# Optimization experiments

Measured on AMD Instinct MI355X. Metric: run time of the kernel, lower is better.

The kernel has to match this reference:

```python
import jax, jax.numpy as jnp
import numpy as np

B, S, D, H, DFF = 4, 2048, 1024, 16, 4096
HD = D // H  # head_dim = 64


def rmsnorm(x, scale, eps=1e-6):
    var = jnp.mean(jnp.square(x), axis=-1, keepdims=True)
    return x * jax.lax.rsqrt(var + eps) * scale


def setup_inputs() -> dict:
    key = jax.random.key(0)
    ks = jax.random.split(key, 16)
    s = 1.0 / np.sqrt(D)
    inp = {
        "x": jax.random.normal(ks[0], (B, S, D), jnp.float32),
        "wq": jax.random.normal(ks[1], (D, D), jnp.float32) * s,
        "bq": jnp.zeros((D,), jnp.float32),
        "wk": jax.random.normal(ks[2], (D, D), jnp.float32) * s,
        "bk": jnp.zeros((D,), jnp.float32),
        "wv": jax.random.normal(ks[3], (D, D), jnp.float32) * s,
        "bv": jnp.zeros((D,), jnp.float32),
        "wbeta": jax.random.normal(ks[4], (D, H), jnp.float32) * s,
        "bbeta": jnp.zeros((H,), jnp.float32),
        "wo": jax.random.normal(ks[5], (D, D), jnp.float32) * s,
        "bo": jnp.zeros((D,), jnp.float32),
        "w1": jax.random.normal(ks[6], (D, DFF), jnp.float32) * s,
        "b1": jnp.zeros((DFF,), jnp.float32),
        "w2": jax.random.normal(ks[7], (DFF, D), jnp.float32) * (1.0 / np.sqrt(DFF)),
        "b2": jnp.zeros((D,), jnp.float32),
        "ln1_scale": jnp.ones((D,), jnp.float32),
        "ln2_scale": jnp.ones((D,), jnp.float32),
    }
    return inp


def gdn_attention(x, wq, bq, wk, bk, wv, bv, wbeta, bbeta, wo, bo):
    b, s, _ = x.shape
    q = (x @ wq + bq).reshape(b, s, H, HD)
    k = (x @ wk + bk).reshape(b, s, H, HD)
    v = (x @ wv + bv).reshape(b, s, H, HD)
    k = k / (jnp.linalg.norm(k, axis=-1, keepdims=True) + 1e-6)
    beta = jax.nn.sigmoid(x @ wbeta + bbeta)[..., None]  # (b, s, H, 1)

    # time-major for scan: (s, b, H, ...)
    q = jnp.transpose(q, (1, 0, 2, 3))
    k = jnp.transpose(k, (1, 0, 2, 3))
    v = jnp.transpose(v, (1, 0, 2, 3))
    beta = jnp.transpose(beta, (1, 0, 2, 3))

    def _step(Sm, inputs):
        q_t, k_t, v_t, beta_t = inputs
        Sk = jnp.einsum('bhde,bhe->bhd', Sm, k_t)
        delta = v_t - Sk
        Sm = Sm + beta_t[..., None] * jnp.einsum('bhd,bhe->bhde', delta, k_t)
        o_t = jnp.einsum('bhde,bhe->bhd', Sm, q_t)
        return Sm, o_t

    S0 = jnp.zeros((b, H, HD, HD), x.dtype)
    _, outputs = jax.lax.scan(_step, S0, (q, k, v, beta))
    outputs = jnp.transpose(outputs, (1, 0, 2, 3)).reshape(b, s, D)
    return outputs @ wo + bo


def reference(x, wq, bq, wk, bk, wv, bv, wbeta, bbeta, wo, bo,
              w1, b1, w2, b2, ln1_scale, ln2_scale):
    residual = x
    h = rmsnorm(x, ln1_scale)
    h = gdn_attention(h, wq, bq, wk, bk, wv, bv, wbeta, bbeta, wo, bo)
    x = h + residual
    residual = x
    h = rmsnorm(x, ln2_scale)
    h = jax.nn.gelu(h @ w1 + b1) @ w2 + b2
    return h + residual
```

## Files before the change

kernel.cpp:

```cpp
#include <hip/hip_runtime.h>

#define DEV __device__ __forceinline__

typedef short bf16x8 __attribute__((ext_vector_type(8)));
typedef float f32x4 __attribute__((ext_vector_type(4)));
typedef unsigned int uint;

#define SBAR()   asm volatile("s_barrier" ::: "memory")
#define WAITV(n) asm volatile("s_waitcnt vmcnt(" #n ")" ::: "memory")
#define WAITL()  asm volatile("s_waitcnt lgkmcnt(0)" ::: "memory")

DEV unsigned short f2b(float f) {
    uint u = __float_as_uint(f);
    u += 0x7fffu + ((u >> 16) & 1u);
    return (unsigned short)(u >> 16);
}
DEV uint packbf2(float a, float b) { return (uint)f2b(a) | ((uint)f2b(b) << 16); }
DEV float b2f(unsigned short s) { return __uint_as_float(((uint)s) << 16); }
DEV float b2f_lo(uint u) { return __uint_as_float(u << 16); }
DEV float b2f_hi(uint u) { return __uint_as_float(u & 0xffff0000u); }

DEV void async_cp16(const void* g, void* l) {
    __builtin_amdgcn_global_load_lds(
        (const __attribute__((address_space(1))) unsigned int*)g,
        (__attribute__((address_space(3))) unsigned int*)l, 16, 0, 0);
}

DEV float quad_sum(float x) {
    x += __int_as_float(__builtin_amdgcn_update_dpp(0, __float_as_int(x), 0xB1, 0xF, 0xF, true));
    x += __int_as_float(__builtin_amdgcn_update_dpp(0, __float_as_int(x), 0x4E, 0xF, 0xF, true));
    return x;
}

DEV float gelu_f(float u) {
    float p = u + 0.044715f * u * u * u;
    float e = __expf(-1.5957691216f * p);
    return __fdividef(u, 1.f + e);
}

DEV void dec8(uint4 p, float* o) {
    o[0] = b2f_lo(p.x); o[1] = b2f_hi(p.x); o[2] = b2f_lo(p.y); o[3] = b2f_hi(p.y);
    o[4] = b2f_lo(p.z); o[5] = b2f_hi(p.z); o[6] = b2f_lo(p.w); o[7] = b2f_hi(p.w);
}

__global__ __launch_bounds__(256) void transpose_cast_k(
    const float* __restrict__ in, unsigned short* __restrict__ out, int K, int N)
{
    __shared__ float tile[32][33];
    const int k0 = blockIdx.x * 32, n0 = blockIdx.y * 32;
    const int tx = threadIdx.x & 31, ty = threadIdx.x >> 5;
#pragma unroll
    for (int i = 0; i < 32; i += 8) {
        int n = n0 + tx;
        tile[ty + i][tx] = (n < N) ? in[(size_t)(k0 + ty + i) * N + n] : 0.0f;
    }
    __syncthreads();
#pragma unroll
    for (int i = 0; i < 32; i += 8) {
        out[(size_t)(n0 + ty + i) * K + (k0 + tx)] = f2b(tile[tx][ty + i]);
    }
}

__global__ void build_bias_k(const float* __restrict__ bq, const float* __restrict__ bk,
                             const float* __restrict__ bv, const float* __restrict__ bb,
                             float* __restrict__ outb)
{
    int i = blockIdx.x * 256 + threadIdx.x;
    if (i >= 3328) return;
    float v = 0.f;
    if (i < 1024)      v = bq[i];
    else if (i < 2048) v = bk[i - 1024];
    else if (i < 3072) v = bv[i - 2048];
    else if (i < 3088) v = bb[i - 3072];
    outb[i] = v;
}

__global__ __launch_bounds__(256) void rmsnorm_cast_k(
    const float* __restrict__ x, const float* __restrict__ scale,
    unsigned short* __restrict__ out)
{
    const int row = blockIdx.x;
    const int t = threadIdx.x;
    const float4 v = *(const float4*)(x + (size_t)row * 1024 + t * 4);
    float ss = v.x * v.x + v.y * v.y + v.z * v.z + v.w * v.w;
#pragma unroll
    for (int off = 1; off < 64; off <<= 1) ss += __shfl_xor(ss, off);
    __shared__ float wsum[4];
    if ((t & 63) == 0) wsum[t >> 6] = ss;
    __syncthreads();
    const float tot = wsum[0] + wsum[1] + wsum[2] + wsum[3];
    const float inv = rsqrtf(tot * (1.0f / 1024.0f) + 1e-6f);
    const float4 sc = *(const float4*)(scale + t * 4);
    uint lo = (uint)f2b(v.x * inv * sc.x) | ((uint)f2b(v.y * inv * sc.y) << 16);
    uint hi = (uint)f2b(v.z * inv * sc.z) | ((uint)f2b(v.w * inv * sc.w) << 16);
    uint2 pkd; pkd.x = lo; pkd.y = hi;
    *(uint2*)(out + (size_t)row * 1024 + t * 4) = pkd;
}

template <bool GELU, bool GUARD>
__global__ __launch_bounds__(512, 2) void gemm256(
    const unsigned short* __restrict__ A, const unsigned short* __restrict__ BT,
    const float* __restrict__ bias, unsigned short* __restrict__ C,
    int Nstride, int Nreal, int K)
{
    __shared__ __align__(16) unsigned short As[4][256 * 32];
    __shared__ __align__(16) unsigned short Bs[4][256 * 32];
    const int tid = threadIdx.x;
    const int wid = tid >> 6;
    const int lane = tid & 63;
    const int l16 = lane & 15, quad = lane >> 4;
    const int wm = wid & 1, wn = wid >> 1;
    const int m0 = blockIdx.x << 8, n0 = blockIdx.y << 8;

    const int srow = (wid << 5) + (lane >> 2);
    const int scol = ((lane & 3) ^ ((lane >> 3) & 3)) << 3;
    const unsigned short* Ag = A + (size_t)(m0 + srow) * K + scol;
    const unsigned short* Bg = BT + (size_t)(n0 + srow) * K + scol;
    const size_t rstep16 = (size_t)16 * K;
    const int ldst = wid << 10;

    f32x4 acc[8][4];
#pragma unroll
    for (int i = 0; i < 8; i++)
#pragma unroll
        for (int j = 0; j < 4; j++) acc[i][j] = (f32x4)0.f;

    const int ksw = (quad ^ ((l16 >> 1) & 3)) << 3;
    const int aoff = ((wm << 7) + l16) * 32 + ksw;
    const int boff = ((wn << 6) + l16) * 32 + ksw;

    const int nt = K >> 5;
    async_cp16(Ag, &As[0][ldst]);
    async_cp16(Ag + rstep16, &As[0][ldst + 512]);
    async_cp16(Bg, &Bs[0][ldst]);
    async_cp16(Bg + rstep16, &Bs[0][ldst + 512]);
    async_cp16(Ag + 32, &As[1][ldst]);
    async_cp16(Ag + 32 + rstep16, &As[1][ldst + 512]);
    async_cp16(Bg + 32, &Bs[1][ldst]);
    async_cp16(Bg + 32 + rstep16, &Bs[1][ldst + 512]);
    WAITV(4);
    SBAR();

    for (int tb = 0; tb < nt; tb += 4) {
#pragma unroll
        for (int u = 0; u < 4; ++u) {
            const int t = tb + u;
            const int pb = (u + 2) & 3;
            const bool st = (t + 2) < nt;
            const size_t kpre = (size_t)(t + 2) << 5;
            bf16x8 af[8], bfr[4];
#pragma unroll
            for (int mi = 0; mi < 8; mi++) af[mi] = *(const bf16x8*)&As[u][aoff + mi * 512];
#pragma unroll
            for (int ni = 0; ni < 4; ni++) bfr[ni] = *(const bf16x8*)&Bs[u][boff + ni * 512];
            if (st) {
                async_cp16(Ag + kpre, &As[pb][ldst]);
                async_cp16(Ag + kpre + rstep16, &As[pb][ldst + 512]);
                async_cp16(Bg + kpre, &Bs[pb][ldst]);
                async_cp16(Bg + kpre + rstep16, &Bs[pb][ldst + 512]);
                WAITV(4);
            } else {
                WAITV(0);
            }
            SBAR();
            __builtin_amdgcn_s_setprio(1);
#pragma unroll
            for (int mi = 0; mi < 8; mi++)
#pragma unroll
                for (int ni = 0; ni < 4; ni++)
                    acc[mi][ni] = __builtin_amdgcn_mfma_f32_16x16x32_bf16(af[mi], bfr[ni], acc[mi][ni], 0, 0, 0);
            __builtin_amdgcn_s_setprio(0);
            SBAR();
        }
    }

    float bv[4];
    const int ccol = n0 + (wn << 6) + l16;
#pragma unroll
    for (int ni = 0; ni < 4; ni++) bv[ni] = bias[ccol + ni * 16];
#pragma unroll
    for (int mi = 0; mi < 8; mi++) {
        const int row = m0 + (wm << 7) + mi * 16 + (quad << 2);
#pragma unroll
        for (int r = 0; r < 4; r++) {
            unsigned short* Crow = C + (size_t)(row + r) * Nstride + ccol;
#pragma unroll
            for (int ni = 0; ni < 4; ni++) {
                float v = acc[mi][ni][r] + bv[ni];
                if (GELU) v = gelu_f(v);
                if (!GUARD || (ccol + ni * 16) < Nreal) Crow[ni * 16] = f2b(v);
            }
        }
    }
}

template <bool ADD>
__global__ __launch_bounds__(512, 2) void gemm128n256(
    const unsigned short* __restrict__ A, const unsigned short* __restrict__ BT,
    const float* __restrict__ bias, const float* __restrict__ add,
    float* __restrict__ C, int N, int K)
{
    __shared__ __align__(16) unsigned short As[4][128 * 32];
    __shared__ __align__(16) unsigned short Bs[4][256 * 32];
    const int tid = threadIdx.x;
    const int wid = tid >> 6;
    const int lane = tid & 63;
    const int l16 = lane & 15, quad = lane >> 4;
    const int wm = wid & 1, wn = wid >> 1;
    const int m0 = blockIdx.x << 7, n0 = blockIdx.y << 8;

    const int arow = (wid << 4) + (lane >> 2);
    const int brow = (wid << 5) + (lane >> 2);
    const int scol = ((lane & 3) ^ ((lane >> 3) & 3)) << 3;
    const unsigned short* Ag = A + (size_t)(m0 + arow) * K + scol;
    const unsigned short* Bg = BT + (size_t)(n0 + brow) * K + scol;
    const size_t rstep16 = (size_t)16 * K;
    const int lda = wid << 9;
    const int ldb = wid << 10;

    f32x4 acc[4][4];
#pragma unroll
    for (int i = 0; i < 4; i++)
#pragma unroll
        for (int j = 0; j < 4; j++) acc[i][j] = (f32x4)0.f;

    const int ksw = (quad ^ ((l16 >> 1) & 3)) << 3;
    const int aoff = ((wm << 6) + l16) * 32 + ksw;
    const int boff = ((wn << 6) + l16) * 32 + ksw;

    const int nt = K >> 5;
    async_cp16(Ag, &As[0][lda]);
    async_cp16(Bg, &Bs[0][ldb]);
    async_cp16(Bg + rstep16, &Bs[0][ldb + 512]);
    async_cp16(Ag + 32, &As[1][lda]);
    async_cp16(Bg + 32, &Bs[1][ldb]);
    async_cp16(Bg + 32 + rstep16, &Bs[1][ldb + 512]);
    WAITV(3);
    SBAR();

    for (int tb = 0; tb < nt; tb += 4) {
#pragma unroll
        for (int u = 0; u < 4; ++u) {
            const int t = tb + u;
            const int pb = (u + 2) & 3;
            const bool st = (t + 2) < nt;
            const size_t kpre = (size_t)(t + 2) << 5;
            bf16x8 af[4], bfr[4];
#pragma unroll
            for (int mi = 0; mi < 4; mi++) af[mi] = *(const bf16x8*)&As[u][aoff + mi * 512];
#pragma unroll
            for (int ni = 0; ni < 4; ni++) bfr[ni] = *(const bf16x8*)&Bs[u][boff + ni * 512];
            if (st) {
                async_cp16(Ag + kpre, &As[pb][lda]);
                async_cp16(Bg + kpre, &Bs[pb][ldb]);
                async_cp16(Bg + kpre + rstep16, &Bs[pb][ldb + 512]);
                WAITV(3);
            } else {
                WAITV(0);
            }
            SBAR();
            __builtin_amdgcn_s_setprio(1);
#pragma unroll
            for (int mi = 0; mi < 4; mi++)
#pragma unroll
                for (int ni = 0; ni < 4; ni++)
                    acc[mi][ni] = __builtin_amdgcn_mfma_f32_16x16x32_bf16(af[mi], bfr[ni], acc[mi][ni], 0, 0, 0);
            __builtin_amdgcn_s_setprio(0);
            SBAR();
        }
    }

    const int ccol = n0 + (wn << 6) + l16;
    float bv[4];
#pragma unroll
    for (int ni = 0; ni < 4; ni++) bv[ni] = bias[ccol + ni * 16];
#pragma unroll
    for (int mi = 0; mi < 4; mi++) {
        const int row = m0 + (wm << 6) + mi * 16 + (quad << 2);
#pragma unroll
        for (int r = 0; r < 4; r++) {
#pragma unroll
            for (int ni = 0; ni < 4; ni++) {
                size_t idx = (size_t)(row + r) * N + ccol + ni * 16;
                float v = acc[mi][ni][r] + bv[ni];
                if (ADD) v += add[idx];
                C[idx] = v;
            }
        }
    }
}


__global__ __launch_bounds__(256) void gdn_prep(
    unsigned short* __restrict__ qkv, unsigned short* __restrict__ Wg,
    unsigned short* __restrict__ ZTg, unsigned short* __restrict__ KTg)
{
    const int chunk = blockIdx.x, bh = blockIdx.y;
    const int b = bh >> 4, h = bh & 15;
    __shared__ float Ks[64 * 68];
    __shared__ float Ws[64 * 65];
    __shared__ float Zs[64 * 65];
    __shared__ float Asl[64 * 65];
    __shared__ float bs[64];
    const int tid = threadIdx.x;
    const int t = tid >> 2, c = tid & 3;
    unsigned short* rowp = qkv + (size_t)(b * 2048 + chunk * 64 + t) * 3200;

    float kn[16];
    {
        uint4 ka = *(const uint4*)(rowp + 1024 + h * 64 + 16 * c);
        uint4 kb = *(const uint4*)(rowp + 1024 + h * 64 + 16 * c + 8);
        dec8(ka, kn); dec8(kb, kn + 8);
    }
    float ss = 0.f;
#pragma unroll
    for (int j = 0; j < 16; j++) ss += kn[j] * kn[j];
    ss = quad_sum(ss);
    const float inv = 1.f / (sqrtf(ss) + 1e-6f);
#pragma unroll
    for (int j = 0; j < 16; j++) kn[j] *= inv;
#pragma unroll
    for (int j = 0; j < 16; j++) Ks[t * 68 + 16 * c + j] = kn[j];
    {
        uint4 p0, p1;
        p0.x = packbf2(kn[0], kn[1]);  p0.y = packbf2(kn[2], kn[3]);
        p0.z = packbf2(kn[4], kn[5]);  p0.w = packbf2(kn[6], kn[7]);
        p1.x = packbf2(kn[8], kn[9]);  p1.y = packbf2(kn[10], kn[11]);
        p1.z = packbf2(kn[12], kn[13]); p1.w = packbf2(kn[14], kn[15]);
        *(uint4*)(rowp + 1024 + h * 64 + 16 * c) = p0;
        *(uint4*)(rowp + 1024 + h * 64 + 16 * c + 8) = p1;
    }
    if (c == 0) bs[t] = 1.f / (1.f + __expf(-b2f(rowp[3072 + h])));
    __syncthreads();

    const float beta = bs[t];
#pragma unroll
    for (int j = 0; j < 16; j++) Ws[t * 65 + 16 * c + j] = beta * kn[j];
    {
        float vv[16];
        uint4 va = *(const uint4*)(rowp + 2048 + h * 64 + 16 * c);
        uint4 vb = *(const uint4*)(rowp + 2048 + h * 64 + 16 * c + 8);
        dec8(va, vv); dec8(vb, vv + 8);
#pragma unroll
        for (int j = 0; j < 16; j++) Zs[t * 65 + 16 * c + j] = beta * vv[j];
    }
    __syncthreads();

    {
        const int tt = tid >> 4, sx = tid & 15;
        float dm[4][4];
#pragma unroll
        for (int i = 0; i < 4; i++)
#pragma unroll
            for (int j = 0; j < 4; j++) dm[i][j] = 0.f;
        for (int d = 0; d < 64; d++) {
            float kt[4], ksv[4];
#pragma unroll
            for (int i = 0; i < 4; i++) kt[i] = Ks[(4 * tt + i) * 68 + d];
#pragma unroll
            for (int j = 0; j < 4; j++) ksv[j] = Ks[(4 * sx + j) * 68 + d];
#pragma unroll
            for (int i = 0; i < 4; i++)
#pragma unroll
                for (int j = 0; j < 4; j++) dm[i][j] += kt[i] * ksv[j];
        }
#pragma unroll
        for (int i = 0; i < 4; i++)
#pragma unroll
            for (int j = 0; j < 4; j++) {
                int T = 4 * tt + i, S_ = 4 * sx + j;
                Asl[T * 65 + S_] = (S_ < T) ? bs[T] * dm[i][j] : 0.f;
            }
    }
    __syncthreads();

    {
        const int wid = tid >> 6, lane = tid & 63;
        for (int qi = 0; qi < 4; qi++) {
            if (qi > 0) {
                const int tb = qi * 16 + wid * 4;
                float aw[4], az[4];
#pragma unroll
                for (int i = 0; i < 4; i++) { aw[i] = Ws[(tb + i) * 65 + lane]; az[i] = Zs[(tb + i) * 65 + lane]; }
                for (int s = 0; s < qi * 16; s++) {
                    float wsv = Ws[s * 65 + lane], zsv = Zs[s * 65 + lane];
#pragma unroll
                    for (int i = 0; i < 4; i++) {
                        float a = Asl[(tb + i) * 65 + s];
                        aw[i] -= a * wsv; az[i] -= a * zsv;
                    }
                }
#pragma unroll
                for (int i = 0; i < 4; i++) { Ws[(tb + i) * 65 + lane] = aw[i]; Zs[(tb + i) * 65 + lane] = az[i]; }
            }
            __syncthreads();
            if (wid == 0) {
                for (int T = qi * 16; T < qi * 16 + 16; T++) {
                    float a_ = Ws[T * 65 + lane];
                    for (int s = qi * 16; s < T; s++) a_ -= Asl[T * 65 + s] * Ws[s * 65 + lane];
                    Ws[T * 65 + lane] = a_;
                }
            } else if (wid == 1) {
                for (int T = qi * 16; T < qi * 16 + 16; T++) {
                    float a_ = Zs[T * 65 + lane];
                    for (int s = qi * 16; s < T; s++) a_ -= Asl[T * 65 + s] * Zs[s * 65 + lane];
                    Zs[T * 65 + lane] = a_;
                }
            }
            __syncthreads();
        }
    }

    const size_t cbase = ((size_t)bh * 32 + chunk) * 4096;
    {
#pragma unroll
        for (int half = 0; half < 2; half++) {
            uint4 w4;
            w4.x = packbf2(Ws[t * 65 + 16 * c + half * 8 + 0], Ws[t * 65 + 16 * c + half * 8 + 1]);
            w4.y = packbf2(Ws[t * 65 + 16 * c + half * 8 + 2], Ws[t * 65 + 16 * c + half * 8 + 3]);
            w4.z = packbf2(Ws[t * 65 + 16 * c + half * 8 + 4], Ws[t * 65 + 16 * c + half * 8 + 5]);
            w4.w = packbf2(Ws[t * 65 + 16 * c + half * 8 + 6], Ws[t * 65 + 16 * c + half * 8 + 7]);
            *(uint4*)(Wg + cbase + (size_t)((2 * c + half) * 64 + t) * 8) = w4;
        }
    }
    {
        const int jj = tid >> 2, tq = tid & 3;
#pragma unroll
        for (int half = 0; half < 2; half++) {
            uint4 z4;
            int i0 = half * 8;
            z4.x = packbf2(Zs[(16 * tq + i0 + 0) * 65 + jj], Zs[(16 * tq + i0 + 1) * 65 + jj]);
            z4.y = packbf2(Zs[(16 * tq + i0 + 2) * 65 + jj], Zs[(16 * tq + i0 + 3) * 65 + jj]);
            z4.z = packbf2(Zs[(16 * tq + i0 + 4) * 65 + jj], Zs[(16 * tq + i0 + 5) * 65 + jj]);
            z4.w = packbf2(Zs[(16 * tq + i0 + 6) * 65 + jj], Zs[(16 * tq + i0 + 7) * 65 + jj]);
            *(uint4*)(ZTg + cbase + (size_t)((2 * tq + half) * 64 + jj) * 8) = z4;
        }
    }
    {
        const int dd = tid >> 2, tq = tid & 3;
#pragma unroll
        for (int half = 0; half < 2; half++) {
            uint4 k4;
            int i0 = half * 8;
            k4.x = packbf2(Ks[(16 * tq + i0 + 0) * 68 + dd], Ks[(16 * tq + i0 + 1) * 68 + dd]);
            k4.y = packbf2(Ks[(16 * tq + i0 + 2) * 68 + dd], Ks[(16 * tq + i0 + 3) * 68 + dd]);
            k4.z = packbf2(Ks[(16 * tq + i0 + 4) * 68 + dd], Ks[(16 * tq + i0 + 5) * 68 + dd]);
            k4.w = packbf2(Ks[(16 * tq + i0 + 6) * 68 + dd], Ks[(16 * tq + i0 + 7) * 68 + dd]);
            *(uint4*)(KTg + cbase + (size_t)((2 * tq + half) * 64 + dd) * 8) = k4;
        }
    }
}

__global__ __launch_bounds__(256, 1) void gdn_prop_mfma(
    const unsigned short* __restrict__ Wg, const unsigned short* __restrict__ KTg,
    const unsigned short* __restrict__ ZTg, unsigned short* __restrict__ Sg,
    unsigned short* __restrict__ YTg)
{
    const int bh = blockIdx.x;
    __shared__ unsigned short WbU[2][4096];
    __shared__ unsigned short KTbU[2][4096];
    __shared__ unsigned short ZTbU[2][4096];
    __shared__ unsigned short SbU[4096];
    const int tid = threadIdx.x;
    const int wid = tid >> 6;
    const int lane = tid & 63;
    const int l16 = lane & 15, quad = lane >> 4;

    f32x4 Sacc[4];
#pragma unroll
    for (int dt = 0; dt < 4; dt++) Sacc[dt] = (f32x4)0.f;

    {
        const size_t cb0 = ((size_t)bh * 32) * 4096;
#pragma unroll
        for (int p = 0; p < 2; p++) {
            const int n = wid * 2 + p;
            async_cp16(Wg + cb0 + n * 512 + lane * 8, &WbU[0][n * 512]);
            async_cp16(KTg + cb0 + n * 512 + lane * 8, &KTbU[0][n * 512]);
            async_cp16(ZTg + cb0 + n * 512 + lane * 8, &ZTbU[0][n * 512]);
        }
    }
    WAITV(0);
    SBAR();

    for (int ch = 0; ch < 32; ch++) {
        const int cur = ch & 1, nxt = cur ^ 1;
        const size_t cbase = ((size_t)bh * 32 + ch) * 4096;
        unsigned short* Wb  = WbU[cur];
        unsigned short* KTb = KTbU[cur];
        unsigned short* ZTb = ZTbU[cur];

        if (ch + 1 < 32) {
            const size_t cbn = cbase + 4096;
#pragma unroll
            for (int p = 0; p < 2; p++) {
                const int n = wid * 2 + p;
                async_cp16(Wg + cbn + n * 512 + lane * 8, &WbU[nxt][n * 512]);
                async_cp16(KTg + cbn + n * 512 + lane * 8, &KTbU[nxt][n * 512]);
                async_cp16(ZTg + cbn + n * 512 + lane * 8, &ZTbU[nxt][n * 512]);
            }
        }
#pragma unroll
        for (int dt = 0; dt < 4; dt++) {
#pragma unroll
            for (int r = 0; r < 4; r++) {
                const int j = wid * 16 + quad * 4 + r;
                SbU[((2 * dt + (l16 >> 3)) * 64 + j) * 8 + (l16 & 7)] = f2b(Sacc[dt][r]);
            }
        }
        WAITL();
        SBAR();

        {
            uint4 sa0 = *(const uint4*)&SbU[tid * 16];
            uint4 sa1 = *(const uint4*)&SbU[tid * 16 + 8];
            *(uint4*)(Sg + cbase + tid * 16) = sa0;
            *(uint4*)(Sg + cbase + tid * 16 + 8) = sa1;
        }

        f32x4 t1[4];
#pragma unroll
        for (int tt = 0; tt < 4; tt++) t1[tt] = (f32x4)0.f;
#pragma unroll
        for (int kh = 0; kh < 2; kh++) {
            const int g = kh * 4 + quad;
            bf16x8 afr = *(const bf16x8*)&SbU[(g * 64 + wid * 16 + l16) * 8];
#pragma unroll
            for (int tt = 0; tt < 4; tt++) {
                bf16x8 bfr = *(const bf16x8*)&Wb[(g * 64 + tt * 16 + l16) * 8];
                t1[tt] = __builtin_amdgcn_mfma_f32_16x16x32_bf16(afr, bfr, t1[tt], 0, 0, 0);
            }
        }
#pragma unroll
        for (int tt = 0; tt < 4; tt++) {
            const int t = tt * 16 + l16;
            const int gb = (t >> 3) * 64;
            unsigned short ybf[4];
#pragma unroll
            for (int r = 0; r < 4; r++) {
                const int j = wid * 16 + quad * 4 + r;
                const float z = b2f(ZTb[(gb + j) * 8 + (t & 7)]);
                ybf[r] = f2b(z - t1[tt][r]);
            }
#pragma unroll
            for (int r = 0; r < 4; r++) {
                const int j = wid * 16 + quad * 4 + r;
                ZTb[(gb + j) * 8 + (t & 7)] = ybf[r];
            }
        }
#pragma unroll
        for (int kh = 0; kh < 2; kh++) {
            const int g = kh * 4 + quad;
            bf16x8 afr = *(const bf16x8*)&ZTb[(g * 64 + wid * 16 + l16) * 8];
#pragma unroll
            for (int dt = 0; dt < 4; dt++) {
                bf16x8 bfr = *(const bf16x8*)&KTb[(g * 64 + dt * 16 + l16) * 8];
                Sacc[dt] = __builtin_amdgcn_mfma_f32_16x16x32_bf16(afr, bfr, Sacc[dt], 0, 0, 0);
            }
        }
#pragma unroll
        for (int pp = 0; pp < 2; pp++) {
            const int p = lane * 2 + pp;
            const int g = p >> 4, jj = p & 15;
            const int off = (g * 64 + wid * 16 + jj) * 8;
            uint4 yv = *(const uint4*)&ZTb[off];
            *(uint4*)(YTg + cbase + off) = yv;
        }
        WAITV(0);
        SBAR();
    }
}

__global__ __launch_bounds__(256) void gdn_out(
    const unsigned short* __restrict__ qkv, const unsigned short* __restrict__ YTg,
    const unsigned short* __restrict__ Sg, unsigned short* __restrict__ attn)
{
    const int chunk = blockIdx.x, bh = blockIdx.y;
    const int b = bh >> 4, h = bh & 15;
    __shared__ unsigned short QbU[8 * 516];
    __shared__ unsigned short KbU[8 * 516];
    __shared__ unsigned short StU[8 * 516];
    __shared__ unsigned short YtU[8 * 516];
    __shared__ unsigned short MhU[8 * 516];
    __shared__ unsigned short MlU[8 * 516];
    const int tid = threadIdx.x;
    const int wid = tid >> 6, lane = tid & 63;
    const int l16 = lane & 15, quad = lane >> 4;
    const size_t cbase = ((size_t)bh * 32 + chunk) * 4096;

    {
        const int t = tid >> 2, c = tid & 3;
        const unsigned short* rowp = qkv + (size_t)(b * 2048 + chunk * 64 + t) * 3200;
        uint4 qa = *(const uint4*)(rowp + h * 64 + 16 * c);
        uint4 qb = *(const uint4*)(rowp + h * 64 + 16 * c + 8);
        uint4 ka = *(const uint4*)(rowp + 1024 + h * 64 + 16 * c);
        uint4 kb = *(const uint4*)(rowp + 1024 + h * 64 + 16 * c + 8);
        *(uint4*)&QbU[(2 * c) * 516 + t * 8]     = qa;
        *(uint4*)&QbU[(2 * c + 1) * 516 + t * 8] = qb;
        *(uint4*)&KbU[(2 * c) * 516 + t * 8]     = ka;
        *(uint4*)&KbU[(2 * c + 1) * 516 + t * 8] = kb;
        const int g = tid >> 5, row = (tid * 2) & 63;
        uint4 s0 = *(const uint4*)(Sg + cbase + tid * 16);
        uint4 s1 = *(const uint4*)(Sg + cbase + tid * 16 + 8);
        *(uint4*)&StU[g * 516 + row * 8]       = s0;
        *(uint4*)&StU[g * 516 + (row + 1) * 8] = s1;
        uint4 y0 = *(const uint4*)(YTg + cbase + tid * 16);
        uint4 y1 = *(const uint4*)(YTg + cbase + tid * 16 + 8);
        *(uint4*)&YtU[g * 516 + row * 8]       = y0;
        *(uint4*)&YtU[g * 516 + (row + 1) * 8] = y1;
    }
    __syncthreads();

    f32x4 m[4], o[4];
#pragma unroll
    for (int i = 0; i < 4; i++) { m[i] = (f32x4)0.f; o[i] = (f32x4)0.f; }

#pragma unroll
    for (int kh = 0; kh < 2; kh++) {
        const int g = kh * 4 + quad;
        bf16x8 afr = *(const bf16x8*)&QbU[g * 516 + (wid * 16 + l16) * 8];
#pragma unroll
        for (int st = 0; st < 4; st++) {
            bf16x8 bk = *(const bf16x8*)&KbU[g * 516 + (st * 16 + l16) * 8];
            m[st] = __builtin_amdgcn_mfma_f32_16x16x32_bf16(afr, bk, m[st], 0, 0, 0);
        }
#pragma unroll
        for (int jt = 0; jt < 4; jt++) {
            bf16x8 bs_ = *(const bf16x8*)&StU[g * 516 + (jt * 16 + l16) * 8];
            o[jt] = __builtin_amdgcn_mfma_f32_16x16x32_bf16(afr, bs_, o[jt], 0, 0, 0);
        }
    }

#pragma unroll
    for (int st = 0; st < 4; st++) {
#pragma unroll
        for (int r = 0; r < 4; r++) {
            const int t = wid * 16 + quad * 4 + r;
            const int s = st * 16 + l16;
            float v = (s <= t) ? m[st][r] : 0.f;
            unsigned short hi = f2b(v);
            unsigned short lo = f2b(v - b2f(hi));
            const int addr = (s >> 3) * 516 + t * 8 + (s & 7);
            MhU[addr] = hi;
            MlU[addr] = lo;
        }
    }
    __syncthreads();

#pragma unroll
    for (int kh = 0; kh < 2; kh++) {
        const int g = kh * 4 + quad;
        bf16x8 ah = *(const bf16x8*)&MhU[g * 516 + (wid * 16 + l16) * 8];
        bf16x8 al = *(const bf16x8*)&MlU[g * 516 + (wid * 16 + l16) * 8];
#pragma unroll
        for (int jt = 0; jt < 4; jt++) {
            bf16x8 by = *(const bf16x8*)&YtU[g * 516 + (jt * 16 + l16) * 8];
            o[jt] = __builtin_amdgcn_mfma_f32_16x16x32_bf16(ah, by, o[jt], 0, 0, 0);
            o[jt] = __builtin_amdgcn_mfma_f32_16x16x32_bf16(al, by, o[jt], 0, 0, 0);
        }
    }

#pragma unroll
    for (int jt = 0; jt < 4; jt++) {
#pragma unroll
        for (int r = 0; r < 4; r++) {
            const int t = wid * 16 + quad * 4 + r;
            attn[(size_t)(b * 2048 + chunk * 64 + t) * 1024 + h * 64 + jt * 16 + l16] = f2b(o[jt][r]);
        }
    }
}

static constexpr size_t OFF_H     = 0;
static constexpr size_t OFF_WQKVT = OFF_H + 16777216;
static constexpr size_t OFF_WOT   = OFF_WQKVT + 6553600;
static constexpr size_t OFF_W1T   = OFF_WOT + 2097152;
static constexpr size_t OFF_W2T   = OFF_W1T + 8388608;
static constexpr size_t OFF_BIAS  = OFF_W2T + 8388608;
static constexpr size_t OFF_QKV   = OFF_BIAS + 16384;
static constexpr size_t OFF_ATTN  = OFF_QKV + 67108864;
static constexpr size_t OFF_Y1    = OFF_ATTN + 16777216;
static constexpr size_t OFF_WG    = OFF_Y1 + 33554432;
static constexpr size_t OFF_YG    = OFF_WG + 16777216;

extern "C" void kernel_launch(void* const* d_in, const int* in_sizes, int n_in,
                              void* d_out, int out_size, void* d_ws, size_t ws_size,
                              hipStream_t stream)
{
    const float* x     = (const float*)d_in[0];
    const float* wq    = (const float*)d_in[1];
    const float* bq    = (const float*)d_in[2];
    const float* wk    = (const float*)d_in[3];
    const float* bk    = (const float*)d_in[4];
    const float* wv    = (const float*)d_in[5];
    const float* bv    = (const float*)d_in[6];
    const float* wbeta = (const float*)d_in[7];
    const float* bbeta = (const float*)d_in[8];
    const float* wo    = (const float*)d_in[9];
    const float* bo    = (const float*)d_in[10];
    const float* w1    = (const float*)d_in[11];
    const float* b1    = (const float*)d_in[12];
    const float* w2    = (const float*)d_in[13];
    const float* b2    = (const float*)d_in[14];
    const float* ln1   = (const float*)d_in[15];
    const float* ln2   = (const float*)d_in[16];

    char* ws = (char*)d_ws;
    unsigned short* hbuf  = (unsigned short*)(ws + OFF_H);
    unsigned short* Sg    = (unsigned short*)(ws + OFF_H);
    unsigned short* wqkvT = (unsigned short*)(ws + OFF_WG);
    unsigned short* woT   = (unsigned short*)(ws + OFF_WOT);
    unsigned short* w1T   = (unsigned short*)(ws + OFF_W1T);
    unsigned short* w2T   = (unsigned short*)(ws + OFF_W2T);
    float*          biasc = (float*)(ws + OFF_BIAS);
    unsigned short* qkvU  = (unsigned short*)(ws + OFF_QKV);
    unsigned short* gbuf  = (unsigned short*)(ws + OFF_QKV);
    unsigned short* attn  = (unsigned short*)(ws + OFF_ATTN);
    float*          y1    = (float*)(ws + OFF_Y1);
    unsigned short* ZTg   = (unsigned short*)(ws + OFF_Y1);
    unsigned short* KTg   = (unsigned short*)(ws + OFF_Y1 + 16777216);
    unsigned short* Wg    = (unsigned short*)(ws + OFF_WG);
    unsigned short* YTg   = (unsigned short*)(ws + OFF_YG);
    float*          out   = (float*)d_out;

    transpose_cast_k<<<dim3(32, 32), 256, 0, stream>>>(wq, wqkvT,               1024, 1024);
    transpose_cast_k<<<dim3(32, 32), 256, 0, stream>>>(wk, wqkvT + 1024 * 1024, 1024, 1024);
    transpose_cast_k<<<dim3(32, 32), 256, 0, stream>>>(wv, wqkvT + 2048 * 1024, 1024, 1024);
    transpose_cast_k<<<dim3(32, 8),  256, 0, stream>>>(wbeta, wqkvT + 3072 * 1024, 1024, 16);
    transpose_cast_k<<<dim3(32, 32), 256, 0, stream>>>(wo, woT, 1024, 1024);
    transpose_cast_k<<<dim3(32, 128), 256, 0, stream>>>(w1, w1T, 1024, 4096);
    transpose_cast_k<<<dim3(128, 32), 256, 0, stream>>>(w2, w2T, 4096, 1024);
    build_bias_k<<<13, 256, 0, stream>>>(bq, bk, bv, bbeta, biasc);

    rmsnorm_cast_k<<<8192, 256, 0, stream>>>(x, ln1, hbuf);
    gemm256<false, true><<<dim3(32, 13), 512, 0, stream>>>(hbuf, wqkvT, biasc, qkvU, 3200, 3200, 1024);
    gdn_prep<<<dim3(32, 64), 256, 0, stream>>>(qkvU, Wg, ZTg, KTg);
    gdn_prop_mfma<<<64, 256, 0, stream>>>(Wg, KTg, ZTg, Sg, YTg);
    gdn_out<<<dim3(32, 64), 256, 0, stream>>>(qkvU, YTg, Sg, attn);
    gemm128n256<true><<<dim3(64, 4), 512, 0, stream>>>(attn, woT, bo, x, y1, 1024, 1024);
    rmsnorm_cast_k<<<8192, 256, 0, stream>>>(y1, ln2, hbuf);
    gemm256<true, false><<<dim3(32, 16), 512, 0, stream>>>(hbuf, w1T, b1, gbuf, 4096, 4096, 1024);
    gemm128n256<true><<<dim3(64, 4), 512, 0, stream>>>(gbuf, w2T, b2, y1, out, 1024, 4096);
}
```

Measured before the change: 596.1 us.

## Switch GEMMs to double-buffered LDS and 128x128 tiles for output projections

The large GEMM goes from a 4-stage, 2-ahead async prefetch pipeline to a 2-stage double buffer: it issues the next tile's loads before computing and waits for them after the MFMAs. This halves LDS use, which may let more blocks fit per CU. The wo and w2 GEMMs are replaced by a 256-thread kernel with 128x128 tiles, doubling the grid to 512 blocks for better CU coverage. In exchange, prefetch distance is shorter, so load latency is exposed more easily, and each iteration still has a barrier.

After: 647.4 us. +8.6%, slower.

```diff
diff --git a/kernel.cpp b/kernel.cpp
--- a/kernel.cpp
+++ b/kernel.cpp
@@ -103,8 +103,8 @@
     const float* __restrict__ bias, unsigned short* __restrict__ C,
     int Nstride, int Nreal, int K)
 {
-    __shared__ __align__(16) unsigned short As[4][256 * 32];
-    __shared__ __align__(16) unsigned short Bs[4][256 * 32];
+    __shared__ __align__(16) unsigned short As[2][256 * 32];
+    __shared__ __align__(16) unsigned short Bs[2][256 * 32];
     const int tid = threadIdx.x;
     const int wid = tid >> 6;
     const int lane = tid & 63;
@@ -134,35 +134,26 @@
     async_cp16(Ag + rstep16, &As[0][ldst + 512]);
     async_cp16(Bg, &Bs[0][ldst]);
     async_cp16(Bg + rstep16, &Bs[0][ldst + 512]);
-    async_cp16(Ag + 32, &As[1][ldst]);
-    async_cp16(Ag + 32 + rstep16, &As[1][ldst + 512]);
-    async_cp16(Bg + 32, &Bs[1][ldst]);
-    async_cp16(Bg + 32 + rstep16, &Bs[1][ldst + 512]);
-    WAITV(4);
+    WAITV(0);
     SBAR();
 
-    for (int tb = 0; tb < nt; tb += 4) {
-#pragma unroll
-        for (int u = 0; u < 4; ++u) {
+    for (int tb = 0; tb < nt; tb += 2) {
+#pragma unroll
+        for (int u = 0; u < 2; ++u) {
             const int t = tb + u;
-            const int pb = (u + 2) & 3;
-            const bool st = (t + 2) < nt;
-            const size_t kpre = (size_t)(t + 2) << 5;
+            const int nb = u ^ 1;
+            if (t + 1 < nt) {
+                const size_t kp = (size_t)(t + 1) << 5;
+                async_cp16(Ag + kp, &As[nb][ldst]);
+                async_cp16(Ag + kp + rstep16, &As[nb][ldst + 512]);
+                async_cp16(Bg + kp, &Bs[nb][ldst]);
+                async_cp16(Bg + kp + rstep16, &Bs[nb][ldst + 512]);
+            }
             bf16x8 af[8], bfr[4];
 #pragma unroll
             for (int mi = 0; mi < 8; mi++) af[mi] = *(const bf16x8*)&As[u][aoff + mi * 512];
 #pragma unroll
             for (int ni = 0; ni < 4; ni++) bfr[ni] = *(const bf16x8*)&Bs[u][boff + ni * 512];
-            if (st) {
-                async_cp16(Ag + kpre, &As[pb][ldst]);
-                async_cp16(Ag + kpre + rstep16, &As[pb][ldst + 512]);
-                async_cp16(Bg + kpre, &Bs[pb][ldst]);
-                async_cp16(Bg + kpre + rstep16, &Bs[pb][ldst + 512]);
-                WAITV(4);
-            } else {
-                WAITV(0);
-            }
-            SBAR();
             __builtin_amdgcn_s_setprio(1);
 #pragma unroll
             for (int mi = 0; mi < 8; mi++)
@@ -170,6 +161,7 @@
                 for (int ni = 0; ni < 4; ni++)
                     acc[mi][ni] = __builtin_amdgcn_mfma_f32_16x16x32_bf16(af[mi], bfr[ni], acc[mi][ni], 0, 0, 0);
             __builtin_amdgcn_s_setprio(0);
+            WAITV(0);
             SBAR();
         }
     }
@@ -195,28 +187,26 @@
 }
 
 template <bool ADD>
-__global__ __launch_bounds__(512, 2) void gemm128n256(
+__global__ __launch_bounds__(256, 2) void gemm128s(
     const unsigned short* __restrict__ A, const unsigned short* __restrict__ BT,
     const float* __restrict__ bias, const float* __restrict__ add,
     float* __restrict__ C, int N, int K)
 {
-    __shared__ __align__(16) unsigned short As[4][128 * 32];
-    __shared__ __align__(16) unsigned short Bs[4][256 * 32];
+    __shared__ __align__(16) unsigned short As[2][128 * 32];
+    __shared__ __align__(16) unsigned short Bs[2][128 * 32];
     const int tid = threadIdx.x;
     const int wid = tid >> 6;
     const int lane = tid & 63;
     const int l16 = lane & 15, quad = lane >> 4;
     const int wm = wid & 1, wn = wid >> 1;
-    const int m0 = blockIdx.x << 7, n0 = blockIdx.y << 8;
-
-    const int arow = (wid << 4) + (lane >> 2);
-    const int brow = (wid << 5) + (lane >> 2);
-    const int scol = ((lane & 3) ^ ((lane >> 3) & 3)) << 3;
-    const unsigned short* Ag = A + (size_t)(m0 + arow) * K + scol;
-    const unsigned short* Bg = BT + (size_t)(n0 + brow) * K + scol;
-    const size_t rstep16 = (size_t)16 * K;
-    const int lda = wid << 9;
-    const int ldb = wid << 10;
+    const int m0 = blockIdx.x << 7, n0 = blockIdx.y << 7;
+
+    const int srow = tid >> 2;
+    const int scol = ((tid & 3) ^ ((tid >> 3) & 3)) << 3;
+    const unsigned short* Ag = A + (size_t)(m0 + srow) * K + scol;
+    const unsigned short* Bg = BT + (size_t)(n0 + srow) * K + scol;
+    const size_t rstep64 = (size_t)64 * K;
+    const int ldst = wid << 9;
 
     f32x4 acc[4][4];
 #pragma unroll
@@ -229,36 +219,30 @@
     const int boff = ((wn << 6) + l16) * 32 + ksw;
 
     const int nt = K >> 5;
-    async_cp16(Ag, &As[0][lda]);
-    async_cp16(Bg, &Bs[0][ldb]);
-    async_cp16(Bg + rstep16, &Bs[0][ldb + 512]);
-    async_cp16(Ag + 32, &As[1][lda]);
-    async_cp16(Bg + 32, &Bs[1][ldb]);
-    async_cp16(Bg + 32 + rstep16, &Bs[1][ldb + 512]);
-    WAITV(3);
+    async_cp16(Ag, &As[0][ldst]);
+    async_cp16(Ag + rstep64, &As[0][2048 + ldst]);
+    async_cp16(Bg, &Bs[0][ldst]);
+    async_cp16(Bg + rstep64, &Bs[0][2048 + ldst]);
+    WAITV(0);
     SBAR();
 
-    for (int tb = 0; tb < nt; tb += 4) {
-#pragma unroll
-        for (int u = 0; u < 4; ++u) {
+    for (int tb = 0; tb < nt; tb += 2) {
+#pragma unroll
+        for (int u = 0; u < 2; ++u) {
             const int t = tb + u;
-            const int pb = (u + 2) & 3;
-            const bool st = (t + 2) < nt;
-            const size_t kpre = (size_t)(t + 2) << 5;
+            const int nb = u ^ 1;
+            if (t + 1 < nt) {
+                const size_t kp = (size_t)(t + 1) << 5;
+                async_cp16(Ag + kp, &As[nb][ldst]);
+                async_cp16(Ag + kp + rstep64, &As[nb][2048 + ldst]);
+                async_cp16(Bg + kp, &Bs[nb][ldst]);
+                async_cp16(Bg + kp + rstep64, &Bs[nb][2048 + ldst]);
+            }
             bf16x8 af[4], bfr[4];
 #pragma unroll
             for (int mi = 0; mi < 4; mi++) af[mi] = *(const bf16x8*)&As[u][aoff + mi * 512];
 #pragma unroll
             for (int ni = 0; ni < 4; ni++) bfr[ni] = *(const bf16x8*)&Bs[u][boff + ni * 512];
-            if (st) {
-                async_cp16(Ag + kpre, &As[pb][lda]);
-                async_cp16(Bg + kpre, &Bs[pb][ldb]);
-                async_cp16(Bg + kpre + rstep16, &Bs[pb][ldb + 512]);
-                WAITV(3);
-            } else {
-                WAITV(0);
-            }
-            SBAR();
             __builtin_amdgcn_s_setprio(1);
 #pragma unroll
             for (int mi = 0; mi < 4; mi++)
@@ -266,6 +250,7 @@
                 for (int ni = 0; ni < 4; ni++)
                     acc[mi][ni] = __builtin_amdgcn_mfma_f32_16x16x32_bf16(af[mi], bfr[ni], acc[mi][ni], 0, 0, 0);
             __builtin_amdgcn_s_setprio(0);
+            WAITV(0);
             SBAR();
         }
     }
@@ -736,8 +721,8 @@
     gdn_prep<<<dim3(32, 64), 256, 0, stream>>>(qkvU, Wg, ZTg, KTg);
     gdn_prop_mfma<<<64, 256, 0, stream>>>(Wg, KTg, ZTg, Sg, YTg);
     gdn_out<<<dim3(32, 64), 256, 0, stream>>>(qkvU, YTg, Sg, attn);
-    gemm128n256<true><<<dim3(64, 4), 512, 0, stream>>>(attn, woT, bo, x, y1, 1024, 1024);
+    gemm128s<true><<<dim3(64, 8), 256, 0, stream>>>(attn, woT, bo, x, y1, 1024, 1024);
     rmsnorm_cast_k<<<8192, 256, 0, stream>>>(y1, ln2, hbuf);
     gemm256<true, false><<<dim3(32, 16), 512, 0, stream>>>(hbuf, w1T, b1, gbuf, 4096, 4096, 1024);
-    gemm128n256<true><<<dim3(64, 4), 512, 0, stream>>>(gbuf, w2T, b2, y1, out, 1024, 4096);
-}
+    gemm128s<true><<<dim3(64, 8), 256, 0, stream>>>(gbuf, w2T, b2, y1, out, 1024, 4096);
+}
```

## Split GDN state propagation across row-slice blocks and merge weight-prep launches

Applied to the files above, without the earlier changes.

The sequential chunk-propagation kernel is split so each (batch,head) is handled by four single-wave blocks, each owning a 16-row slice of the state, instead of one 256-thread block. This removes all block-level barriers inside the serial chunk loop and spreads the work over four times as many CUs. The cost is that every block now loads the full W and K^T chunk tiles itself, which raises global and LDS traffic. Separately, the seven weight transpose-cast launches and the bias build are fused into one kernel to cut launch overhead.

Result: faster. 576.2 us (-3.3%).

```diff
diff --git a/kernel.cpp b/kernel.cpp
--- a/kernel.cpp
+++ b/kernel.cpp
@@ -43,11 +43,40 @@
     o[4] = b2f_lo(p.z); o[5] = b2f_hi(p.z); o[6] = b2f_lo(p.w); o[7] = b2f_hi(p.w);
 }
 
-__global__ __launch_bounds__(256) void transpose_cast_k(
-    const float* __restrict__ in, unsigned short* __restrict__ out, int K, int N)
+__global__ __launch_bounds__(256) void weight_prep_k(
+    const float* __restrict__ wq, const float* __restrict__ wk,
+    const float* __restrict__ wv, const float* __restrict__ wbeta,
+    const float* __restrict__ wo, const float* __restrict__ w1,
+    const float* __restrict__ w2,
+    unsigned short* __restrict__ wqkvT, unsigned short* __restrict__ woT,
+    unsigned short* __restrict__ w1T, unsigned short* __restrict__ w2T,
+    const float* __restrict__ bq, const float* __restrict__ bk,
+    const float* __restrict__ bv, const float* __restrict__ bb,
+    float* __restrict__ biasc)
 {
+    const int id = blockIdx.x;
+    if (id >= 12544) {
+        int i = (id - 12544) * 256 + threadIdx.x;
+        if (i >= 3328) return;
+        float v = 0.f;
+        if (i < 1024)      v = bq[i];
+        else if (i < 2048) v = bk[i - 1024];
+        else if (i < 3072) v = bv[i - 2048];
+        else if (i < 3088) v = bb[i - 3072];
+        biasc[i] = v;
+        return;
+    }
+    const float* in; unsigned short* out; int K, N, KT, loc;
+    if (id < 1024)      { in = wq;    out = wqkvT;               K = 1024; N = 1024; KT = 32;  loc = id; }
+    else if (id < 2048) { in = wk;    out = wqkvT + 1024 * 1024; K = 1024; N = 1024; KT = 32;  loc = id - 1024; }
+    else if (id < 3072) { in = wv;    out = wqkvT + 2048 * 1024; K = 1024; N = 1024; KT = 32;  loc = id - 2048; }
+    else if (id < 3328) { in = wbeta; out = wqkvT + 3072 * 1024; K = 1024; N = 16;   KT = 32;  loc = id - 3072; }
+    else if (id < 4352) { in = wo;    out = woT;                 K = 1024; N = 1024; KT = 32;  loc = id - 3328; }
+    else if (id < 8448) { in = w1;    out = w1T;                 K = 1024; N = 4096; KT = 32;  loc = id - 4352; }
+    else                { in = w2;    out = w2T;                 K = 4096; N = 1024; KT = 128; loc = id - 8448; }
+    const int k0 = (loc % KT) * 32, n0 = (loc / KT) * 32;
+
     __shared__ float tile[32][33];
-    const int k0 = blockIdx.x * 32, n0 = blockIdx.y * 32;
     const int tx = threadIdx.x & 31, ty = threadIdx.x >> 5;
 #pragma unroll
     for (int i = 0; i < 32; i += 8) {
@@ -59,20 +88,6 @@
     for (int i = 0; i < 32; i += 8) {
         out[(size_t)(n0 + ty + i) * K + (k0 + tx)] = f2b(tile[tx][ty + i]);
     }
-}
-
-__global__ void build_bias_k(const float* __restrict__ bq, const float* __restrict__ bk,
-                             const float* __restrict__ bv, const float* __restrict__ bb,
-                             float* __restrict__ outb)
-{
-    int i = blockIdx.x * 256 + threadIdx.x;
-    if (i >= 3328) return;
-    float v = 0.f;
-    if (i < 1024)      v = bq[i];
-    else if (i < 2048) v = bk[i - 1024];
-    else if (i < 3072) v = bv[i - 2048];
-    else if (i < 3088) v = bb[i - 3072];
-    outb[i] = v;
 }
 
 __global__ __launch_bounds__(256) void rmsnorm_cast_k(
@@ -451,19 +466,18 @@
     }
 }
 
-__global__ __launch_bounds__(256, 1) void gdn_prop_mfma(
+__global__ __launch_bounds__(64, 1) void gdn_prop_mfma(
     const unsigned short* __restrict__ Wg, const unsigned short* __restrict__ KTg,
     const unsigned short* __restrict__ ZTg, unsigned short* __restrict__ Sg,
     unsigned short* __restrict__ YTg)
 {
     const int bh = blockIdx.x;
-    __shared__ unsigned short WbU[2][4096];
-    __shared__ unsigned short KTbU[2][4096];
-    __shared__ unsigned short ZTbU[2][4096];
-    __shared__ unsigned short SbU[4096];
-    const int tid = threadIdx.x;
-    const int wid = tid >> 6;
-    const int lane = tid & 63;
+    const int jb = blockIdx.y << 4;
+    __shared__ unsigned short Wb[2][4096];
+    __shared__ unsigned short KTb[2][4096];
+    __shared__ unsigned short ZTb[2][1024];
+    __shared__ unsigned short Sb[1024];
+    const int lane = threadIdx.x;
     const int l16 = lane & 15, quad = lane >> 4;
 
     f32x4 Sacc[4];
@@ -473,49 +487,46 @@
     {
         const size_t cb0 = ((size_t)bh * 32) * 4096;
 #pragma unroll
-        for (int p = 0; p < 2; p++) {
-            const int n = wid * 2 + p;
-            async_cp16(Wg + cb0 + n * 512 + lane * 8, &WbU[0][n * 512]);
-            async_cp16(KTg + cb0 + n * 512 + lane * 8, &KTbU[0][n * 512]);
-            async_cp16(ZTg + cb0 + n * 512 + lane * 8, &ZTbU[0][n * 512]);
-        }
+        for (int p = 0; p < 8; p++) async_cp16(Wg + cb0 + p * 512 + lane * 8, &Wb[0][p * 512]);
+#pragma unroll
+        for (int p = 0; p < 8; p++) async_cp16(KTg + cb0 + p * 512 + lane * 8, &KTb[0][p * 512]);
+#pragma unroll
+        for (int c = 0; c < 2; c++)
+            async_cp16(ZTg + cb0 + (size_t)((c * 4 + (lane >> 4)) * 64 + jb + (lane & 15)) * 8,
+                       &ZTb[0][c * 512]);
     }
     WAITV(0);
-    SBAR();
 
     for (int ch = 0; ch < 32; ch++) {
         const int cur = ch & 1, nxt = cur ^ 1;
         const size_t cbase = ((size_t)bh * 32 + ch) * 4096;
-        unsigned short* Wb  = WbU[cur];
-        unsigned short* KTb = KTbU[cur];
-        unsigned short* ZTb = ZTbU[cur];
 
         if (ch + 1 < 32) {
             const size_t cbn = cbase + 4096;
 #pragma unroll
-            for (int p = 0; p < 2; p++) {
-                const int n = wid * 2 + p;
-                async_cp16(Wg + cbn + n * 512 + lane * 8, &WbU[nxt][n * 512]);
-                async_cp16(KTg + cbn + n * 512 + lane * 8, &KTbU[nxt][n * 512]);
-                async_cp16(ZTg + cbn + n * 512 + lane * 8, &ZTbU[nxt][n * 512]);
-            }
-        }
+            for (int p = 0; p < 8; p++) async_cp16(Wg + cbn + p * 512 + lane * 8, &Wb[nxt][p * 512]);
+#pragma unroll
+            for (int p = 0; p < 8; p++) async_cp16(KTg + cbn + p * 512 + lane * 8, &KTb[nxt][p * 512]);
+#pragma unroll
+            for (int c = 0; c < 2; c++)
+                async_cp16(ZTg + cbn + (size_t)((c * 4 + (lane >> 4)) * 64 + jb + (lane & 15)) * 8,
+                           &ZTb[nxt][c * 512]);
+        }
+
 #pragma unroll
         for (int dt = 0; dt < 4; dt++) {
 #pragma unroll
             for (int r = 0; r < 4; r++) {
-                const int j = wid * 16 + quad * 4 + r;
-                SbU[((2 * dt + (l16 >> 3)) * 64 + j) * 8 + (l16 & 7)] = f2b(Sacc[dt][r]);
-            }
-        }
-        WAITL();
-        SBAR();
-
+                const int lj = quad * 4 + r;
+                Sb[((2 * dt + (l16 >> 3)) * 16 + lj) * 8 + (l16 & 7)] = f2b(Sacc[dt][r]);
+            }
+        }
         {
-            uint4 sa0 = *(const uint4*)&SbU[tid * 16];
-            uint4 sa1 = *(const uint4*)&SbU[tid * 16 + 8];
-            *(uint4*)(Sg + cbase + tid * 16) = sa0;
-            *(uint4*)(Sg + cbase + tid * 16 + 8) = sa1;
+            const int gd = lane >> 3, lj0 = (lane & 7) * 2;
+            uint4 s0 = *(const uint4*)&Sb[lane * 16];
+            uint4 s1 = *(const uint4*)&Sb[lane * 16 + 8];
+            *(uint4*)(Sg + cbase + (size_t)(gd * 64 + jb + lj0) * 8) = s0;
+            *(uint4*)(Sg + cbase + (size_t)(gd * 64 + jb + lj0 + 1) * 8) = s1;
         }
 
         f32x4 t1[4];
@@ -524,50 +535,47 @@
 #pragma unroll
         for (int kh = 0; kh < 2; kh++) {
             const int g = kh * 4 + quad;
-            bf16x8 afr = *(const bf16x8*)&SbU[(g * 64 + wid * 16 + l16) * 8];
+            bf16x8 afr = *(const bf16x8*)&Sb[(g * 16 + l16) * 8];
 #pragma unroll
             for (int tt = 0; tt < 4; tt++) {
-                bf16x8 bfr = *(const bf16x8*)&Wb[(g * 64 + tt * 16 + l16) * 8];
+                bf16x8 bfr = *(const bf16x8*)&Wb[cur][(g * 64 + tt * 16 + l16) * 8];
                 t1[tt] = __builtin_amdgcn_mfma_f32_16x16x32_bf16(afr, bfr, t1[tt], 0, 0, 0);
             }
         }
 #pragma unroll
         for (int tt = 0; tt < 4; tt++) {
             const int t = tt * 16 + l16;
-            const int gb = (t >> 3) * 64;
             unsigned short ybf[4];
 #pragma unroll
             for (int r = 0; r < 4; r++) {
-                const int j = wid * 16 + quad * 4 + r;
-                const float z = b2f(ZTb[(gb + j) * 8 + (t & 7)]);
+                const int lj = quad * 4 + r;
+                const float z = b2f(ZTb[cur][((t >> 3) * 16 + lj) * 8 + (t & 7)]);
                 ybf[r] = f2b(z - t1[tt][r]);
             }
 #pragma unroll
             for (int r = 0; r < 4; r++) {
-                const int j = wid * 16 + quad * 4 + r;
-                ZTb[(gb + j) * 8 + (t & 7)] = ybf[r];
+                const int lj = quad * 4 + r;
+                ZTb[cur][((t >> 3) * 16 + lj) * 8 + (t & 7)] = ybf[r];
             }
         }
 #pragma unroll
         for (int kh = 0; kh < 2; kh++) {
             const int g = kh * 4 + quad;
-            bf16x8 afr = *(const bf16x8*)&ZTb[(g * 64 + wid * 16 + l16) * 8];
+            bf16x8 afr = *(const bf16x8*)&ZTb[cur][(g * 16 + l16) * 8];
 #pragma unroll
             for (int dt = 0; dt < 4; dt++) {
-                bf16x8 bfr = *(const bf16x8*)&KTb[(g * 64 + dt * 16 + l16) * 8];
+                bf16x8 bfr = *(const bf16x8*)&KTb[cur][(g * 64 + dt * 16 + l16) * 8];
                 Sacc[dt] = __builtin_amdgcn_mfma_f32_16x16x32_bf16(afr, bfr, Sacc[dt], 0, 0, 0);
             }
         }
-#pragma unroll
-        for (int pp = 0; pp < 2; pp++) {
-            const int p = lane * 2 + pp;
-            const int g = p >> 4, jj = p & 15;
-            const int off = (g * 64 + wid * 16 + jj) * 8;
-            uint4 yv = *(const uint4*)&ZTb[off];
-            *(uint4*)(YTg + cbase + off) = yv;
+        {
+            const int gt = lane >> 3, lj0 = (lane & 7) * 2;
+            uint4 y0 = *(const uint4*)&ZTb[cur][lane * 16];
+            uint4 y1 = *(const uint4*)&ZTb[cur][lane * 16 + 8];
+            *(uint4*)(YTg + cbase + (size_t)(gt * 64 + jb + lj0) * 8) = y0;
+            *(uint4*)(YTg + cbase + (size_t)(gt * 64 + jb + lj0 + 1) * 8) = y1;
         }
         WAITV(0);
-        SBAR();
     }
 }
 
@@ -722,19 +730,14 @@
     unsigned short* YTg   = (unsigned short*)(ws + OFF_YG);
     float*          out   = (float*)d_out;
 
-    transpose_cast_k<<<dim3(32, 32), 256, 0, stream>>>(wq, wqkvT,               1024, 1024);
-    transpose_cast_k<<<dim3(32, 32), 256, 0, stream>>>(wk, wqkvT + 1024 * 1024, 1024, 1024);
-    transpose_cast_k<<<dim3(32, 32), 256, 0, stream>>>(wv, wqkvT + 2048 * 1024, 1024, 1024);
-    transpose_cast_k<<<dim3(32, 8),  256, 0, stream>>>(wbeta, wqkvT + 3072 * 1024, 1024, 16);
-    transpose_cast_k<<<dim3(32, 32), 256, 0, stream>>>(wo, woT, 1024, 1024);
-    transpose_cast_k<<<dim3(32, 128), 256, 0, stream>>>(w1, w1T, 1024, 4096);
-    transpose_cast_k<<<dim3(128, 32), 256, 0, stream>>>(w2, w2T, 4096, 1024);
-    build_bias_k<<<13, 256, 0, stream>>>(bq, bk, bv, bbeta, biasc);
+    weight_prep_k<<<12557, 256, 0, stream>>>(wq, wk, wv, wbeta, wo, w1, w2,
+                                             wqkvT, woT, w1T, w2T,
+                                             bq, bk, bv, bbeta, biasc);
 
     rmsnorm_cast_k<<<8192, 256, 0, stream>>>(x, ln1, hbuf);
     gemm256<false, true><<<dim3(32, 13), 512, 0, stream>>>(hbuf, wqkvT, biasc, qkvU, 3200, 3200, 1024);
     gdn_prep<<<dim3(32, 64), 256, 0, stream>>>(qkvU, Wg, ZTg, KTg);
-    gdn_prop_mfma<<<64, 256, 0, stream>>>(Wg, KTg, ZTg, Sg, YTg);
+    gdn_prop_mfma<<<dim3(64, 4), 64, 0, stream>>>(Wg, KTg, ZTg, Sg, YTg);
     gdn_out<<<dim3(32, 64), 256, 0, stream>>>(qkvU, YTg, Sg, attn);
     gemm128n256<true><<<dim3(64, 4), 512, 0, stream>>>(attn, woT, bo, x, y1, 1024, 1024);
     rmsnorm_cast_k<<<8192, 256, 0, stream>>>(y1, ln2, hbuf);
```
